# Kernel optimization log

Hardware: AMD Instinct MI355X
Metric: run time of the kernel (lower is better)

Reference implementation:

```python
import jax, jax.numpy as jnp
import numpy as np

L = 8          # layers_num
G = 2 * L + 1  # grid side = 17
NH = 30        # n_hiper
D = 768
N = 4096       # ray samples


def setup_inputs() -> dict:
    key = jax.random.key(0)
    k1, k2, k3 = jax.random.split(key, 3)
    # coords must be in [-L, L) so shifted indices floor+1/ceil+1 stay in-bounds
    samples = jax.random.uniform(k1, (N, 3), minval=-float(L), maxval=float(L) - 1e-3)
    last_point = jax.random.uniform(k2, (3,), minval=-float(L), maxval=float(L) - 1e-3)
    embeddings = jax.random.normal(k3, (G, G, G, NH + 1, D), dtype=jnp.float32)
    return {"samples": samples, "last_point": last_point, "embeddings": embeddings}


def _interpolate(emb, samples):
    """Vectorized port of Text3DSpaceAll.interpolate for all N samples.
    emb: (G,G,G,NH+1,D); samples: (N,3). Returns (N, NH+1, D)."""
    Gs = emb.shape[0]
    p = samples + L                       # shift into [0, G-1)
    f = jnp.floor(p)
    c = jnp.ceil(p)
    d = p - f                             # fractional parts (same as pre-shift)
    fx, fy, fz = f[:, 0].astype(jnp.int32), f[:, 1].astype(jnp.int32), f[:, 2].astype(jnp.int32)
    cy, cz = c[:, 1].astype(jnp.int32), c[:, 2].astype(jnp.int32)
    dx, dy, dz = d[:, 0], d[:, 1], d[:, 2]

    def w(a):  # broadcast per-sample scalar over (NH+1, D)
        return a[:, None, None]

    def clip(i):
        return jnp.clip(i, 0, Gs - 1)

    def line(iy, iz):
        # 2-4 point stencil along x with boundary-dependent count
        g = lambda ix: emb[clip(ix), iy, iz]          # gather -> (N, NH+1, D)
        m_lo = (fx > 0).astype(dx.dtype)
        m_hi = (fx + 2 < Gs).astype(dx.dtype)
        out = (g(fx) * w(2.0 - dx) + g(fx + 1) * w(1.0 + dx)
               + g(fx - 1) * w((1.0 - dx) * m_lo)
               + g(fx + 2) * w(dx * m_hi))
        cnt = 2.0 + m_lo + m_hi
        return out / w(cnt)

    def plane(iz):
        m_lo = (fy > 0).astype(dy.dtype)
        m_hi = (fy + 2 < Gs).astype(dy.dtype)
        out = (line(fy, iz) * w(2.0 - dy) + line(cy, iz) * w(1.0 + dy)
               + line(clip(fy - 1), iz) * w((1.0 - dy) * m_lo)
               + line(clip(cy + 1), iz) * w(dy * m_hi))
        cnt = 2.0 + m_lo + m_hi
        return out / w(cnt)

    m_lo = (fz > 0).astype(dz.dtype)
    m_hi = (fz + 2 < Gs).astype(dz.dtype)
    out = (plane(fz) * w(2.0 - dz) + plane(cz) * w(1.0 + dz)
           + plane(clip(fz - 1)) * w((1.0 - dz) * m_lo)
           + plane(clip(cz + 1)) * w(dz * m_hi))
    cnt = 2.0 + m_lo + m_hi
    return out / w(cnt)


def reference(samples, last_point, embeddings):
    n_hiper = embeddings.shape[3] - 1
    interp = _interpolate(embeddings, samples)          # (N, NH+1, D)
    emb = interp[:, :n_hiper]                           # (N, NH, D)
    density = jax.nn.relu(interp[:, n_hiper])           # (N, D)
    # distance from each sample to the next (last one to last_point)
    nxt = jnp.concatenate([samples[1:], last_point[None]], axis=0)
    dists = jnp.linalg.norm(samples - nxt, axis=-1)     # (N,)
    sd = density * dists[:, None]                       # (N, D)
    # exclusive cumulative optical depth -> transmittance
    csum = jnp.cumsum(sd, axis=0)
    excl = jnp.concatenate([jnp.zeros_like(sd[:1]), csum[:-1]], axis=0)
    T = jnp.exp(-excl)
    alpha = 1.0 - jnp.exp(-sd)
    wgt = T * alpha                                     # (N, D)
    return jnp.einsum('nd,nhd->hd', wgt, emb)           # (NH, D)
```

## Files before the change

kernel.cpp:

```cpp
#include <hip/hip_runtime.h>
#include <math.h>

#define LL 8
#define G 17
#define NH 30
#define D 768
#define N 4096
#define CH 31
#define CELLS (G*G*G)
#define CSTRIDE (CH*D)
#define NBIN 16
#define CPG 32
#define NCHUNK ((CELLS+CPG-1)/CPG)

__device__ __forceinline__ int iclip(int i){ return i<0?0:(i>G-1?G-1:i); }

__global__ void k_prep(const float* __restrict__ samples, const float* __restrict__ last_point,
                       float* __restrict__ wxyz, int* __restrict__ ixyz,
                       float* __restrict__ dist, int* __restrict__ sampleBin,
                       int* __restrict__ binCount){
    int s = blockIdx.x*blockDim.x + threadIdx.x;
    if (s >= N) return;
    float x0 = samples[s*3+0], y0 = samples[s*3+1], z0 = samples[s*3+2];
    float p[3] = {x0 + (float)LL, y0 + (float)LL, z0 + (float)LL};
    float fv[3], cv[3], dv[3]; int fi[3], ci[3];
    for (int a=0;a<3;a++){
        fv[a]=floorf(p[a]); cv[a]=ceilf(p[a]); dv[a]=p[a]-fv[a];
        fi[a]=(int)fv[a]; ci[a]=(int)cv[a];
    }
    {
        int fx=fi[0]; float dx=dv[0];
        float mlo=(fx>0)?1.f:0.f, mhi=(fx+2<G)?1.f:0.f;
        float cnt=2.f+mlo+mhi;
        float w[4]={(1.f-dx)*mlo/cnt,(2.f-dx)/cnt,(1.f+dx)/cnt,dx*mhi/cnt};
        int id[4]={iclip(fx-1),iclip(fx),iclip(fx+1),iclip(fx+2)};
        for(int i=0;i<4;i++){ wxyz[s*12+i]=w[i]; ixyz[s*12+i]=id[i]; }
    }
    {
        int fy=fi[1], cy=ci[1]; float dy=dv[1];
        float mlo=(fy>0)?1.f:0.f, mhi=(fy+2<G)?1.f:0.f;
        float cnt=2.f+mlo+mhi;
        float w[4]={(1.f-dy)*mlo/cnt,(2.f-dy)/cnt,(1.f+dy)/cnt,dy*mhi/cnt};
        int id[4]={iclip(fy-1),iclip(fy),iclip(cy),iclip(cy+1)};
        for(int i=0;i<4;i++){ wxyz[s*12+4+i]=w[i]; ixyz[s*12+4+i]=id[i]; }
    }
    {
        int fz=fi[2], cz=ci[2]; float dz=dv[2];
        float mlo=(fz>0)?1.f:0.f, mhi=(fz+2<G)?1.f:0.f;
        float cnt=2.f+mlo+mhi;
        float w[4]={(1.f-dz)*mlo/cnt,(2.f-dz)/cnt,(1.f+dz)/cnt,dz*mhi/cnt};
        int id[4]={iclip(fz-1),iclip(fz),iclip(cz),iclip(cz+1)};
        for(int i=0;i<4;i++){ wxyz[s*12+8+i]=w[i]; ixyz[s*12+8+i]=id[i]; }
    }
    float nx,ny,nz;
    if (s < N-1){ nx=samples[(s+1)*3+0]; ny=samples[(s+1)*3+1]; nz=samples[(s+1)*3+2]; }
    else        { nx=last_point[0];      ny=last_point[1];      nz=last_point[2]; }
    float ddx=x0-nx, ddy=y0-ny, ddz=z0-nz;
    dist[s]=sqrtf(ddx*ddx+ddy*ddy+ddz*ddz);
    int bx=min(max(fi[0],0),NBIN-1), by=min(max(fi[1],0),NBIN-1), bz=min(max(fi[2],0),NBIN-1);
    int bin=(bz*NBIN+by)*NBIN+bx;
    sampleBin[s]=bin;
    atomicAdd(&binCount[bin],1);
}

__global__ void k_binscan(const int* __restrict__ binCount, int* __restrict__ binStart,
                          int* __restrict__ binCursor){
    __shared__ int sh[256];
    __shared__ int srun;
    int t = threadIdx.x;
    if (t==0) srun=0;
    __syncthreads();
    for (int base=0; base<NBIN*NBIN*NBIN; base+=256){
        int v = binCount[base+t];
        sh[t]=v; __syncthreads();
        for (int off=1; off<256; off<<=1){
            int u = (t>=off)? sh[t-off] : 0;
            __syncthreads();
            sh[t]+=u;
            __syncthreads();
        }
        int incl = sh[t];
        int st = srun + incl - v;
        binStart[base+t]=st; binCursor[base+t]=st;
        __syncthreads();
        if (t==255) srun += incl;
        __syncthreads();
    }
}

__global__ void k_scatter(const int* __restrict__ sampleBin, int* __restrict__ binCursor,
                          int* __restrict__ binned){
    int s = blockIdx.x*blockDim.x + threadIdx.x;
    if (s>=N) return;
    int b=sampleBin[s];
    int pos=atomicAdd(&binCursor[b],1);
    binned[pos]=s;
}

__global__ __launch_bounds__(192) void k_density(const float* __restrict__ emb,
                       const float* __restrict__ wxyz, const int* __restrict__ ixyz,
                       const int* __restrict__ binned,
                       float* __restrict__ density){
    int b = blockIdx.x;
    int s = binned[((b & 7) << 9) | (b >> 3)];
    int t = threadIdx.x;
    __shared__ float w[12]; __shared__ int idx[12];
    if (t<12){ w[t]=wxyz[s*12+t]; idx[t]=ixyz[s*12+t]; }
    __syncthreads();
    float4 acc = make_float4(0.f,0.f,0.f,0.f);
    for (int i=0;i<4;i++){
        float wx=w[i]; if (wx==0.f) continue; int X=idx[i];
        for (int j=0;j<4;j++){
            float wxy=wx*w[4+j]; if (wxy==0.f) continue; int Y=idx[4+j];
            for (int k=0;k<4;k++){
                float www=wxy*w[8+k]; if (www==0.f) continue; int Z=idx[8+k];
                const float4* p = (const float4*)(emb + (size_t)((X*G+Y)*G+Z)*CSTRIDE + NH*D);
                float4 v = p[t];
                acc.x += www*v.x; acc.y += www*v.y; acc.z += www*v.z; acc.w += www*v.w;
            }
        }
    }
    ((float4*)(density + (size_t)s*D))[t] = acc;
}

__global__ void k_transpose(const float* __restrict__ in, float* __restrict__ out,
                            int R, int C){
    __shared__ float tile[64][65];
    int tx=threadIdx.x, ty=threadIdx.y;
    int c0=blockIdx.x*64, r0=blockIdx.y*64;
    #pragma unroll
    for (int k=0;k<16;k++){
        int r=r0+ty+k*4;
        tile[ty+k*4][tx] = in[(size_t)r*C + c0 + tx];
    }
    __syncthreads();
    #pragma unroll
    for (int k=0;k<16;k++){
        int c=c0+ty+k*4;
        out[(size_t)c*R + r0 + tx] = tile[tx][ty+k*4];
    }
}

#define SIDX(n) ((n) + ((n)>>4))
__global__ __launch_bounds__(256) void k_scan(const float* __restrict__ density_t,
                       const float* __restrict__ dist, float* __restrict__ wgt_t){
    __shared__ float buf[4096 + 256];
    __shared__ float wtot[4];
    int t = threadIdx.x;
    int d = blockIdx.x;
    const float* col = density_t + (size_t)d*N;
    float* out = wgt_t + (size_t)d*N;
    #pragma unroll
    for (int i=0;i<16;i++){
        int n = i*256 + t;
        buf[SIDX(n)] = fmaxf(col[n], 0.f) * dist[n];
    }
    __syncthreads();
    int lane = t & 63, wave = t >> 6;
    float vals[16]; float sum = 0.f;
    #pragma unroll
    for (int j=0;j<16;j++){ vals[j] = buf[SIDX(t*16+j)]; sum += vals[j]; }
    float x = sum;
    #pragma unroll
    for (int off=1; off<64; off<<=1){
        float u = __shfl_up(x, (unsigned)off, 64);
        if (lane >= off) x += u;
    }
    if (lane == 63) wtot[wave] = x;
    float thread_excl = x - sum;
    __syncthreads();
    float wexcl = 0.f;
    for (int w2=0; w2<4; w2++) if (w2 < wave) wexcl += wtot[w2];
    float run = wexcl + thread_excl;
    #pragma unroll
    for (int j=0;j<16;j++){
        float sd = vals[j];
        run += sd;
        buf[SIDX(t*16+j)] = expf(sd-run) - expf(-run);
    }
    __syncthreads();
    #pragma unroll
    for (int i=0;i<16;i++){
        int n = i*256 + t;
        out[n] = buf[SIDX(n)];
    }
}

#define MAXS 1024
__global__ __launch_bounds__(192) void k_accumA(const float* __restrict__ wgt,
                       const float* __restrict__ wxyz, const int* __restrict__ ixyz,
                       const int* __restrict__ binStart, const int* __restrict__ binCount,
                       const int* __restrict__ binned, float* __restrict__ A){
    int b = blockIdx.x;
    int c = (b & 7) * 615 + (b >> 3);
    if (c >= CELLS) return;
    int t = threadIdx.x;
    int x=c/(G*G); int rem=c-x*G*G; int y=rem/G; int z=rem-y*G;
    __shared__ int   ls[MAXS];
    __shared__ float lw[MAXS];
    __shared__ int   lcount;
    if (t==0) lcount = 0;
    __syncthreads();
    int bx0=max(0,x-2), bx1=min(NBIN-1,x+1);
    int by0=max(0,y-2), by1=min(NBIN-1,y+1);
    int bz0=max(0,z-2), bz1=min(NBIN-1,z+1);
    int nx=bx1-bx0+1, ny=by1-by0+1, nz=bz1-bz0+1;
    int nb = nx*ny*nz;
    for (int bi=t; bi<nb; bi+=192){
        int bxo = bi % nx; int r2 = bi / nx;
        int byo = r2 % ny; int bzo = r2 / ny;
        int bin = ((bz0+bzo)*NBIN + (by0+byo))*NBIN + (bx0+bxo);
        int st = binStart[bin], cnt = binCount[bin];
        for (int q=0;q<cnt;q++){
            int s = binned[st+q];
            const float* w = wxyz + (size_t)s*12;
            const int* id  = ixyz + (size_t)s*12;
            float px=0.f,py=0.f,pz=0.f;
            #pragma unroll
            for (int i=0;i<4;i++){
                px += (id[i]  ==x)? w[i]  :0.f;
                py += (id[4+i]==y)? w[4+i]:0.f;
                pz += (id[8+i]==z)? w[8+i]:0.f;
            }
            float wt = px*py*pz;
            if (wt != 0.f){
                int pos = atomicAdd(&lcount, 1);
                if (pos < MAXS){ ls[pos]=s; lw[pos]=wt; }
            }
        }
    }
    __syncthreads();
    int m = min(lcount, MAXS);
    float4 acc = make_float4(0.f,0.f,0.f,0.f);
    for (int i=0;i<m;i++){
        int s = ls[i]; float wt = lw[i];
        float4 v = ((const float4*)(wgt + (size_t)s*D))[t];
        acc.x += wt*v.x; acc.y += wt*v.y; acc.z += wt*v.z; acc.w += wt*v.w;
    }
    ((float4*)(A + (size_t)c*D))[t] = acc;
}

__global__ __launch_bounds__(256) void k_out(const float* __restrict__ emb,
                      const float* __restrict__ A, float* __restrict__ partial){
    int t=threadIdx.x;
    int d=blockIdx.y*256+t;
    int chunk=blockIdx.x;
    int c0=chunk*CPG;
    int c1=min(CELLS,c0+CPG);
    float acc[NH];
    #pragma unroll
    for (int h=0;h<NH;h++) acc[h]=0.f;
    for (int c=c0;c<c1;c++){
        float a=A[(size_t)c*D+d];
        const float* e=emb+(size_t)c*CSTRIDE+d;
        #pragma unroll
        for (int h=0;h<NH;h++) acc[h]+=a*e[h*D];
    }
    float* pr = partial + (size_t)chunk*NH*D + d;
    #pragma unroll
    for (int h=0;h<NH;h++) pr[h*D] = acc[h];
}

__global__ __launch_bounds__(256) void k_reduce(const float* __restrict__ partial,
                       float* __restrict__ out){
    int i = blockIdx.x*256 + threadIdx.x;
    if (i >= NH*D) return;
    float s = 0.f;
    for (int c=0;c<NCHUNK;c++) s += partial[(size_t)c*NH*D + i];
    out[i] = s;
}

extern "C" void kernel_launch(void* const* d_in, const int* in_sizes, int n_in,
                              void* d_out, int out_size, void* d_ws, size_t ws_size,
                              hipStream_t stream){
    const float* samples   = (const float*)d_in[0];
    const float* last_point= (const float*)d_in[1];
    const float* emb       = (const float*)d_in[2];
    char* ws=(char*)d_ws;
    float* wxyz     =(float*)(ws + 0);
    int*   ixyz     =(int*)  (ws + 196608);
    float* dist     =(float*)(ws + 393216);
    int*   sampleBin=(int*)  (ws + 409600);
    int*   binCount =(int*)  (ws + 425984);
    int*   binStart =(int*)  (ws + 442368);
    int*   binCursor=(int*)  (ws + 458752);
    int*   binned   =(int*)  (ws + 475136);
    float* density  =(float*)(ws + 524288);
    float* density_t=(float*)(ws + 524288 + 12582912);
    float* wgt_t    =(float*)(ws + 524288 + 2*12582912);
    float* wgt      = density;
    float* A        =(float*)(ws + 524288 + 3*12582912);
    float* partial  =(float*)(ws + 524288 + 3*12582912 + 15093504);

    hipMemsetAsync(binCount, 0, 4096*sizeof(int), stream);

    k_prep   <<<N/256, 256, 0, stream>>>(samples, last_point, wxyz, ixyz, dist, sampleBin, binCount);
    k_binscan<<<1, 256, 0, stream>>>(binCount, binStart, binCursor);
    k_scatter<<<N/256, 256, 0, stream>>>(sampleBin, binCursor, binned);
    k_density<<<N, 192, 0, stream>>>(emb, wxyz, ixyz, binned, density);
    dim3 tb(64,4);
    k_transpose<<<dim3(D/64, N/64), tb, 0, stream>>>(density, density_t, N, D);
    k_scan   <<<D, 256, 0, stream>>>(density_t, dist, wgt_t);
    k_transpose<<<dim3(N/64, D/64), tb, 0, stream>>>(wgt_t, wgt, D, N);
    k_accumA <<<8*615, 192, 0, stream>>>(wgt, wxyz, ixyz, binStart, binCount, binned, A);
    k_out    <<<dim3(NCHUNK, D/256), 256, 0, stream>>>(emb, A, partial);
    k_reduce <<<(NH*D+255)/256, 256, 0, stream>>>(partial, (float*)d_out);
}
```

Baseline: 749.8 us.

## Vectorize k_out over heads, split reduction with atomics, flatten density stencil

k_out now gives each block one chunk of 16 cells and a 10-head slice, with float4 loads per thread instead of 30 scalar accumulators over 256 columns. This gives more blocks and wider memory transactions on the dominant streaming pass over the embedding table. k_reduce splits the chunk sum across 4 y-blocks and combines them with float atomics into a zeroed output. k_density precomputes the list of non-zero stencil taps in shared memory so the gather loop can unroll. The cost is a larger partial buffer, atomic contention, and a summation order that is no longer deterministic.

```diff
diff --git a/kernel.cpp b/kernel.cpp
--- a/kernel.cpp
+++ b/kernel.cpp
@@ -10,7 +10,7 @@
 #define CELLS (G*G*G)
 #define CSTRIDE (CH*D)
 #define NBIN 16
-#define CPG 32
+#define CPG 16
 #define NCHUNK ((CELLS+CPG-1)/CPG)
 
 __device__ __forceinline__ int iclip(int i){ return i<0?0:(i>G-1?G-1:i); }
@@ -105,20 +105,29 @@
     int s = binned[((b & 7) << 9) | (b >> 3)];
     int t = threadIdx.x;
     __shared__ float w[12]; __shared__ int idx[12];
+    __shared__ float lw[64]; __shared__ int loff[64];
+    __shared__ int lcnt;
     if (t<12){ w[t]=wxyz[s*12+t]; idx[t]=ixyz[s*12+t]; }
-    __syncthreads();
+    if (t==0) lcnt=0;
+    __syncthreads();
+    if (t < 64){
+        int i = t>>4, j = (t>>2)&3, k = t&3;
+        float www = w[i]*w[4+j]*w[8+k];
+        if (www != 0.f){
+            int pos = atomicAdd(&lcnt, 1);
+            lw[pos]   = www;
+            loff[pos] = ((idx[i]*G+idx[4+j])*G+idx[8+k])*CSTRIDE + NH*D;
+        }
+    }
+    __syncthreads();
+    int m = lcnt;
     float4 acc = make_float4(0.f,0.f,0.f,0.f);
-    for (int i=0;i<4;i++){
-        float wx=w[i]; if (wx==0.f) continue; int X=idx[i];
-        for (int j=0;j<4;j++){
-            float wxy=wx*w[4+j]; if (wxy==0.f) continue; int Y=idx[4+j];
-            for (int k=0;k<4;k++){
-                float www=wxy*w[8+k]; if (www==0.f) continue; int Z=idx[8+k];
-                const float4* p = (const float4*)(emb + (size_t)((X*G+Y)*G+Z)*CSTRIDE + NH*D);
-                float4 v = p[t];
-                acc.x += www*v.x; acc.y += www*v.y; acc.z += www*v.z; acc.w += www*v.w;
-            }
-        }
+    #pragma unroll 4
+    for (int q=0;q<m;q++){
+        const float4* p = (const float4*)(emb + (size_t)loff[q]);
+        float4 v = p[t];
+        float www = lw[q];
+        acc.x += www*v.x; acc.y += www*v.y; acc.z += www*v.z; acc.w += www*v.w;
     }
     ((float4*)(density + (size_t)s*D))[t] = acc;
 }
@@ -240,34 +249,48 @@
     ((float4*)(A + (size_t)c*D))[t] = acc;
 }
 
-__global__ __launch_bounds__(256) void k_out(const float* __restrict__ emb,
+__global__ __launch_bounds__(192) void k_out(const float* __restrict__ emb,
                       const float* __restrict__ A, float* __restrict__ partial){
-    int t=threadIdx.x;
-    int d=blockIdx.y*256+t;
-    int chunk=blockIdx.x;
-    int c0=chunk*CPG;
-    int c1=min(CELLS,c0+CPG);
-    float acc[NH];
-    #pragma unroll
-    for (int h=0;h<NH;h++) acc[h]=0.f;
+    int t = threadIdx.x;
+    int chunk = blockIdx.x;
+    int h0 = blockIdx.y * 10;
+    int c0 = chunk*CPG;
+    int c1 = min(CELLS, c0+CPG);
+    float4 acc[10];
+    #pragma unroll
+    for (int h=0;h<10;h++) acc[h]=make_float4(0.f,0.f,0.f,0.f);
     for (int c=c0;c<c1;c++){
-        float a=A[(size_t)c*D+d];
-        const float* e=emb+(size_t)c*CSTRIDE+d;
+        float4 a = ((const float4*)(A + (size_t)c*D))[t];
+        const float* ebase = emb + (size_t)c*CSTRIDE + (size_t)h0*D;
         #pragma unroll
-        for (int h=0;h<NH;h++) acc[h]+=a*e[h*D];
-    }
-    float* pr = partial + (size_t)chunk*NH*D + d;
-    #pragma unroll
-    for (int h=0;h<NH;h++) pr[h*D] = acc[h];
+        for (int h=0;h<10;h++){
+            float4 v = ((const float4*)(ebase + (size_t)h*D))[t];
+            acc[h].x += a.x*v.x; acc[h].y += a.y*v.y;
+            acc[h].z += a.z*v.z; acc[h].w += a.w*v.w;
+        }
+    }
+    float* pr = partial + (size_t)chunk*NH*D + (size_t)h0*D;
+    #pragma unroll
+    for (int h=0;h<10;h++)
+        ((float4*)(pr + (size_t)h*D))[t] = acc[h];
 }
 
 __global__ __launch_bounds__(256) void k_reduce(const float* __restrict__ partial,
                        float* __restrict__ out){
     int i = blockIdx.x*256 + threadIdx.x;
-    if (i >= NH*D) return;
-    float s = 0.f;
-    for (int c=0;c<NCHUNK;c++) s += partial[(size_t)c*NH*D + i];
-    out[i] = s;
+    if (i >= NH*D/4) return;
+    int cbeg = blockIdx.y * 77;
+    int cend = min(NCHUNK, cbeg + 77);
+    float4 s = make_float4(0.f,0.f,0.f,0.f);
+    #pragma unroll 4
+    for (int c=cbeg;c<cend;c++){
+        float4 v = ((const float4*)(partial + (size_t)c*NH*D))[i];
+        s.x+=v.x; s.y+=v.y; s.z+=v.z; s.w+=v.w;
+    }
+    atomicAdd(&out[i*4+0], s.x);
+    atomicAdd(&out[i*4+1], s.y);
+    atomicAdd(&out[i*4+2], s.z);
+    atomicAdd(&out[i*4+3], s.w);
 }
 
 extern "C" void kernel_launch(void* const* d_in, const int* in_sizes, int n_in,
@@ -293,6 +316,7 @@
     float* partial  =(float*)(ws + 524288 + 3*12582912 + 15093504);
 
     hipMemsetAsync(binCount, 0, 4096*sizeof(int), stream);
+    hipMemsetAsync(d_out, 0, NH*D*sizeof(float), stream);
 
     k_prep   <<<N/256, 256, 0, stream>>>(samples, last_point, wxyz, ixyz, dist, sampleBin, binCount);
     k_binscan<<<1, 256, 0, stream>>>(binCount, binStart, binCursor);
@@ -303,6 +327,6 @@
     k_scan   <<<D, 256, 0, stream>>>(density_t, dist, wgt_t);
     k_transpose<<<dim3(N/64, D/64), tb, 0, stream>>>(wgt_t, wgt, D, N);
     k_accumA <<<8*615, 192, 0, stream>>>(wgt, wxyz, ixyz, binStart, binCount, binned, A);
-    k_out    <<<dim3(NCHUNK, D/256), 256, 0, stream>>>(emb, A, partial);
-    k_reduce <<<(NH*D+255)/256, 256, 0, stream>>>(partial, (float*)d_out);
-}
+    k_out    <<<dim3(NCHUNK, 3), 192, 0, stream>>>(emb, A, partial);
+    k_reduce <<<dim3((NH*D/4+255)/256, 4), 256, 0, stream>>>(partial, (float*)d_out);
+}
```

Measured after the change: 746.5 us. About the same (-0.4%).
